# Optimization experiments

Measured on AMD Instinct MI355X. Metric: run time of the kernel, lower is better.

Reference implementation:

```python
import jax, jax.numpy as jnp
import numpy as np

N_USERS = 65536
N_ENT = 8192
C = 64
N_REL = 16
E = 1000000
NNZ = 1000000
LAMBDA_COEFF = 0.5
EPS = 1e-12


def setup_inputs() -> dict:
    key = jax.random.key(0)
    ks = jax.random.split(key, 8)
    return {
        "user_emb": jax.random.normal(ks[0], (N_USERS, C), jnp.float32) * 0.1,
        "entity_emb": jax.random.normal(ks[1], (N_ENT, C), jnp.float32) * 0.1,
        "weight": jax.random.normal(ks[2], (N_REL - 1, C), jnp.float32) * 0.1,
        "edge_index": jax.random.randint(ks[3], (2, E), 0, N_ENT, dtype=jnp.int32),
        "edge_type": jax.random.randint(ks[4], (E,), 1, N_REL, dtype=jnp.int32),
        "interact_rows": jax.random.randint(ks[5], (NNZ,), 0, N_USERS, dtype=jnp.int32),
        "interact_cols": jax.random.randint(ks[6], (NNZ,), 0, N_ENT, dtype=jnp.int32),
        "interact_vals": jax.random.uniform(ks[7], (NNZ,), jnp.float32),
        "n_hops": 2,
        "topk": 10,
    }


def _l2_normalize(x):
    # F.normalize(p=2, dim=1) with eps=1e-12
    n = jnp.linalg.norm(x, axis=-1, keepdims=True)
    return x / jnp.maximum(n, EPS)


def _build_adj_dense(context, topk):
    # cosine-sim kNN graph + symmetric normalization, returned dense [n, n]
    n = context.shape[0]
    cn = context / jnp.linalg.norm(context, axis=-1, keepdims=True)
    sim = cn @ cn.T                                  # [n, n]
    knn_val, knn_ind = jax.lax.top_k(sim, topk)      # [n, k]
    rowsum = knn_val.sum(-1)                         # sparse rowsum per row
    d = rowsum ** -0.5                               # D^{-1/2}
    vals = d[:, None] * knn_val * d[knn_ind]         # D^-1/2 A D^-1/2 values
    rows = jnp.broadcast_to(jnp.arange(n)[:, None], (n, topk))
    return jnp.zeros((n, n), context.dtype).at[rows, knn_ind].add(vals)


def _aggregate(entity_emb, user_emb, head, tail, edge_type,
               interact_rows, interact_cols, interact_vals, weight):
    rel = weight[edge_type - 1]                      # [E, C]
    neigh = entity_emb[tail] * rel                   # [E, C]
    # per-edge attention: (||h*r||_2 * ||t*r||_2)^2  -> scalar per edge
    s = (jnp.linalg.norm(entity_emb[head] * rel, axis=1)
         * jnp.linalg.norm(neigh, axis=1)) ** 2      # [E]
    # scatter_softmax over edges grouped by head
    smax = jax.ops.segment_max(s, head, num_segments=N_ENT)
    ex = jnp.exp(s - smax[head])
    denom = jax.ops.segment_sum(ex, head, num_segments=N_ENT)
    w = ex / denom[head]                             # [E]
    entity_agg = jax.ops.segment_sum(neigh * w[:, None], head, num_segments=N_ENT)
    # user_agg = interact_mat @ entity_emb (sparse COO mm)
    user_agg = jax.ops.segment_sum(interact_vals[:, None] * entity_emb[interact_cols],
                                   interact_rows, num_segments=N_USERS)
    score = jax.nn.softmax(user_emb @ weight.T, axis=-1)   # [n_users, n_rel-1]
    user_agg = user_agg + (score @ weight) * user_agg
    return entity_agg, user_agg


def reference(user_emb, entity_emb, weight, edge_index, edge_type,
              interact_rows, interact_cols, interact_vals, n_hops, topk):
    head, tail = edge_index[0], edge_index[1]
    origin_item_adj = _build_adj_dense(entity_emb, topk)
    entity_res = entity_emb
    user_res = user_emb
    ent, usr = entity_emb, user_emb
    for _ in range(n_hops):
        ent, usr = _aggregate(ent, usr, head, tail, edge_type,
                              interact_rows, interact_cols, interact_vals, weight)
        ent = _l2_normalize(ent)
        usr = _l2_normalize(usr)
        entity_res = entity_res + ent
        user_res = user_res + usr
    item_adj = (1.0 - LAMBDA_COEFF) * _build_adj_dense(entity_res, topk) \
               + LAMBDA_COEFF * origin_item_adj
    return entity_res, user_res, item_adj
```

## Files before the change

### kernel.cpp

```cpp
#include <hip/hip_runtime.h>
#include <math.h>
#include <float.h>

#define N_USERS 65536
#define N_ENT   8192
#define CDIM    64
#define N_RELM1 15
#define E_EDGES 1000000
#define NNZV    1000000
#define TOPK    10
#define NCAND   12
#define EPSN    1e-12f

typedef float f32x4 __attribute__((ext_vector_type(4)));
typedef short short8 __attribute__((ext_vector_type(8)));

__device__ inline unsigned umaxu(unsigned a, unsigned b){ return a > b ? a : b; }
__device__ inline unsigned uminu(unsigned a, unsigned b){ return a < b ? a : b; }

__device__ inline float wred_sum(float v){
#pragma unroll
  for (int m = 32; m; m >>= 1) v += __shfl_xor(v, m, 64);
  return v;
}
__device__ inline float wred_max(float v){
#pragma unroll
  for (int m = 32; m; m >>= 1) v = fmaxf(v, __shfl_xor(v, m, 64));
  return v;
}

__device__ inline unsigned bf16_rne(float x){
  unsigned u = __float_as_uint(x);
  return (u + 0x7FFFu + ((u >> 16) & 1u)) >> 16;
}

__global__ void k_rownorm_split(const float* __restrict__ x, float* __restrict__ cn,
                                short* __restrict__ hi_p, short* __restrict__ lo_p, int n){
  int w = (blockIdx.x * blockDim.x + threadIdx.x) >> 6;
  int k = threadIdx.x & 63;
  if (w >= n) return;
  float v = x[w * CDIM + k];
  float ss = wred_sum(v * v);
  float cv = v / sqrtf(ss);
  cn[w * CDIM + k] = cv;
  unsigned h = bf16_rne(cv);
  float hf = __uint_as_float(h << 16);
  unsigned l2 = bf16_rne(cv - hf);
  int T = w >> 4, c = w & 15;
  int f = k >> 5, q = (k >> 3) & 3, j = k & 7;
  size_t a = ((size_t)(T * 2 + f) * 64 + q * 16 + c) * 8 + j;
  hi_p[a] = (short)h;
  lo_p[a] = (short)l2;
}

__global__ __launch_bounds__(256) void k_sim_topk(const short* __restrict__ hi_p,
                                                  const short* __restrict__ lo_p,
                                                  unsigned* __restrict__ keys){
  const int tid = threadIdx.x;
  const int w = tid >> 6, l = tid & 63;
  const int c = l & 15, q = l >> 4;
  const int rowset = (w >> 1) << 4;
  const int half = w & 1;
  const int cy = blockIdx.y;
  const int row0 = blockIdx.x * 32 + rowset;
  const int R = row0 >> 4;

  const short8* H8 = (const short8*)hi_p;
  const short8* L8 = (const short8*)lo_p;

  const short8 a_hi0 = H8[(size_t)R * 128 + l];
  const short8 a_hi1 = H8[(size_t)R * 128 + 64 + l];
  const short8 a_lo0 = L8[(size_t)R * 128 + l];
  const short8 a_lo1 = L8[(size_t)R * 128 + 64 + l];

  unsigned key[4][8];
#pragma unroll
  for (int s = 0; s < 4; ++s)
#pragma unroll
    for (int t = 0; t < 8; ++t) key[s][t] = 0u;

  const f32x4 z4 = {0.f, 0.f, 0.f, 0.f};
  const int bt = cy * 256 + half * 128;
#pragma unroll 2
  for (int lt = 0; lt < 128; ++lt){
    const size_t bo = (size_t)(bt + lt) * 128 + l;
    short8 b_hi0 = H8[bo];
    short8 b_hi1 = H8[bo + 64];
    short8 b_lo0 = L8[bo];
    short8 b_lo1 = L8[bo + 64];
    f32x4 p0 = __builtin_amdgcn_mfma_f32_16x16x32_bf16(a_hi0, b_hi0, z4, 0, 0, 0);
    f32x4 p1 = __builtin_amdgcn_mfma_f32_16x16x32_bf16(a_hi0, b_lo0, z4, 0, 0, 0);
    f32x4 p2 = __builtin_amdgcn_mfma_f32_16x16x32_bf16(a_lo0, b_hi0, z4, 0, 0, 0);
    p0 = __builtin_amdgcn_mfma_f32_16x16x32_bf16(a_hi1, b_hi1, p0, 0, 0, 0);
    p1 = __builtin_amdgcn_mfma_f32_16x16x32_bf16(a_hi1, b_lo1, p1, 0, 0, 0);
    p2 = __builtin_amdgcn_mfma_f32_16x16x32_bf16(a_lo1, b_hi1, p2, 0, 0, 0);
#pragma unroll
    for (int s = 0; s < 4; ++s){
      float v = p0[s] + p1[s] + p2[s];
      unsigned u = __float_as_uint(v);
      unsigned kk = ((u ^ (unsigned)(((int)u >> 31) | 0x80000000)) & 0xFFFFFF00u) | (unsigned)lt;
#pragma unroll
      for (int i = 7; i >= 1; --i)
        key[s][i] = umaxu(uminu(key[s][i - 1], kk), key[s][i]);
      key[s][0] = umaxu(key[s][0], kk);
    }
  }

#pragma unroll
  for (int s = 0; s < 4; ++s){
    int grow = row0 + 4 * q + s;
    unsigned* kp = keys + ((size_t)grow * 64 + (size_t)(cy * 32 + half * 16 + c)) * 8;
    ((uint4*)kp)[0] = (uint4){key[s][0], key[s][1], key[s][2], key[s][3]};
    ((uint4*)kp)[1] = (uint4){key[s][4], key[s][5], key[s][6], key[s][7]};
  }
}

__global__ __launch_bounds__(256) void k_refine(const float* __restrict__ cn,
                                                const unsigned* __restrict__ keys,
                                                float* __restrict__ kv, int* __restrict__ ki,
                                                float* __restrict__ dvec){
  int row = blockIdx.x * 4 + (threadIdx.x >> 6);
  int l = threadIdx.x & 63;
  const unsigned* kp = keys + ((size_t)row * 64 + l) * 8;
  uint4 k0 = ((const uint4*)kp)[0], k1 = ((const uint4*)kp)[1];
  unsigned kk0 = k0.x, kk1 = k0.y, kk2 = k0.z, kk3 = k0.w;
  unsigned kk4 = k1.x, kk5 = k1.y, kk6 = k1.z, kk7 = k1.w;
  const int cbase = (l >> 5) * 4096 + ((l >> 4) & 1) * 2048 + (l & 15);

  int ji[NCAND];
#pragma unroll
  for (int t = 0; t < NCAND; ++t){
    unsigned bk = kk0;
    int myc = cbase + (int)(kk0 & 0xFFu) * 16;
    int bc = myc;
#pragma unroll
    for (int m = 32; m; m >>= 1){
      unsigned ok = (unsigned)__shfl_xor((int)bk, m, 64);
      int oc = __shfl_xor(bc, m, 64);
      if (ok > bk || (ok == bk && oc < bc)){ bk = ok; bc = oc; }
    }
    if (kk0 == bk && myc == bc){
      kk0 = kk1; kk1 = kk2; kk2 = kk3; kk3 = kk4; kk4 = kk5; kk5 = kk6; kk6 = kk7; kk7 = 0u;
    }
    ji[t] = bc;
  }

  float v = cn[(size_t)row * CDIM + l];
  float dv[NCAND];
#pragma unroll
  for (int t = 0; t < NCAND; ++t)
    dv[t] = wred_sum(v * cn[(size_t)ji[t] * CDIM + l]);

  unsigned used = 0;
  float rs = 0.f;
  for (int k = 0; k < TOPK; ++k){
    float bv = -FLT_MAX; int bi = 0x7FFFFFFF; int bs = 0;
#pragma unroll
    for (int t = 0; t < NCAND; ++t){
      if (used & (1u << t)) continue;
      if (dv[t] > bv || (dv[t] == bv && ji[t] < bi)){ bv = dv[t]; bi = ji[t]; bs = t; }
    }
    used |= 1u << bs; rs += bv;
    if (l == 0){ kv[(size_t)row * TOPK + k] = bv; ki[(size_t)row * TOPK + k] = bi; }
  }
  if (l == 0) dvec[row] = 1.0f / sqrtf(rs);
}

__global__ void k_hist(const int* __restrict__ keys, int* __restrict__ deg, int n){
  int e = blockIdx.x * blockDim.x + threadIdx.x;
  if (e < n) atomicAdd(&deg[keys[e]], 1);
}
__global__ __launch_bounds__(1024) void k_scan_local(const int* __restrict__ deg,
                                                     int* __restrict__ out,
                                                     int* __restrict__ part){
  __shared__ int sh[1024];
  int tid = threadIdx.x, g = blockIdx.x * 1024 + tid;
  int v = deg[g];
  sh[tid] = v; __syncthreads();
  for (int off = 1; off < 1024; off <<= 1){
    int t = (tid >= off) ? sh[tid - off] : 0;
    __syncthreads();
    sh[tid] += t;
    __syncthreads();
  }
  out[g] = sh[tid] - v;
  if (tid == 1023) part[blockIdx.x] = sh[1023];
}
__global__ void k_scan_part(int* __restrict__ part, int* __restrict__ total_out, int nb){
  int tid = threadIdx.x;
  int v = (tid < nb) ? part[tid] : 0;
  int orig = v;
  for (int off = 1; off < 64; off <<= 1){
    int t = __shfl_up(v, off, 64);
    if (tid >= off) v += t;
  }
  if (tid < nb) part[tid] = v - orig;
  if (tid == 63) *total_out = v;
}
__global__ __launch_bounds__(1024) void k_scan_add(int* __restrict__ out, const int* __restrict__ part){
  int g = blockIdx.x * 1024 + threadIdx.x;
  out[g] += part[blockIdx.x];
}
__global__ void k_scatter_graph(const int* __restrict__ head, const int* __restrict__ tail,
                                const int* __restrict__ etype, const int* __restrict__ rowptr,
                                int* __restrict__ cnt, int* __restrict__ pack, int n){
  int e = blockIdx.x * blockDim.x + threadIdx.x;
  if (e >= n) return;
  int h = head[e];
  int pos = rowptr[h] + atomicAdd(&cnt[h], 1);
  pack[pos] = tail[e] | ((etype[e] - 1) << 16);
}
__global__ void k_scatter_int(const int* __restrict__ rows, const int* __restrict__ cols,
                              const float* __restrict__ vals, const int* __restrict__ rowptr,
                              int* __restrict__ cnt, int* __restrict__ ocol,
                              float* __restrict__ oval, int n){
  int e = blockIdx.x * blockDim.x + threadIdx.x;
  if (e >= n) return;
  int r = rows[e];
  int pos = rowptr[r] + atomicAdd(&cnt[r], 1);
  ocol[pos] = cols[e];
  oval[pos] = vals[e];
}

__global__ __launch_bounds__(256) void k_normsq(const float* __restrict__ ent,
                                                const float* __restrict__ wmat,
                                                float* __restrict__ nsq){
  __shared__ float wl[N_RELM1 * CDIM];
  int tid = threadIdx.x;
  for (int t = tid; t < N_RELM1 * CDIM; t += 256) wl[t] = wmat[t];
  __syncthreads();
  int i = blockIdx.x * 4 + (tid >> 6);
  int lane = tid & 63;
  float v = ent[(size_t)i * CDIM + lane];
  float out = 0.f;
  for (int r = 0; r < N_RELM1; ++r){
    float t = v * wl[r * CDIM + lane];
    float ss = wred_sum(t * t);
    if (lane == r) out = ss;
  }
  if (lane < N_RELM1) nsq[i * N_RELM1 + lane] = out;
}

__global__ __launch_bounds__(256) void k_entity_hop(const float* __restrict__ ent_cur,
                                                    const float* __restrict__ nsq,
                                                    const float* __restrict__ wmat,
                                                    const int* __restrict__ rowptr,
                                                    const int* __restrict__ pack,
                                                    float* __restrict__ ent_next,
                                                    float* __restrict__ res, int hop0){
  __shared__ float wl[N_RELM1 * CDIM];
  int tid = threadIdx.x;
  for (int t = tid; t < N_RELM1 * CDIM; t += 256) wl[t] = wmat[t];
  __syncthreads();
  int i = blockIdx.x * 4 + (tid >> 6);
  int lane = tid & 63;
  int beg = rowptr[i], end = rowptr[i + 1];

  float sm = 0.f;
  for (int p = beg + lane; p < end; p += 64){
    int pk = pack[p]; int t = pk & 0xFFFF; int r = pk >> 16;
    sm = fmaxf(sm, nsq[i * N_RELM1 + r] * nsq[t * N_RELM1 + r]);
  }
  sm = wred_max(sm);

  float acc = 0.f, denom = 0.f;
  for (int p = beg; p < end; ++p){
    int pk = pack[p]; int t = pk & 0xFFFF; int r = pk >> 16;
    float s = nsq[i * N_RELM1 + r] * nsq[t * N_RELM1 + r];
    float e = expf(s - sm);
    denom += e;
    acc = fmaf(e * wl[r * CDIM + lane], ent_cur[(size_t)t * CDIM + lane], acc);
  }
  float agg = (end > beg) ? acc / denom : 0.f;
  float nrm = sqrtf(wred_sum(agg * agg));
  float out = agg / fmaxf(nrm, EPSN);
  if (hop0){
    ent_next[(size_t)i * CDIM + lane] = out;
    res[(size_t)i * CDIM + lane] = ent_cur[(size_t)i * CDIM + lane] + out;
  } else {
    res[(size_t)i * CDIM + lane] += out;
  }
}

__global__ __launch_bounds__(256) void k_user_hop(const float* __restrict__ base,
                                                  const float* __restrict__ ent_cur,
                                                  const float* __restrict__ wmat,
                                                  const int* __restrict__ rowptr,
                                                  const int* __restrict__ cols,
                                                  const float* __restrict__ vals,
                                                  float* __restrict__ res, int hop0){
  __shared__ float wl[N_RELM1 * CDIM];
  int tid = threadIdx.x;
  for (int t = tid; t < N_RELM1 * CDIM; t += 256) wl[t] = wmat[t];
  __syncthreads();
  int u = blockIdx.x * 4 + (tid >> 6);
  int lane = tid & 63;
  float bv = base[(size_t)u * CDIM + lane];
  float rprev = hop0 ? bv : res[(size_t)u * CDIM + lane];
  float uv = hop0 ? bv : (rprev - bv);

  float dr[N_RELM1];
#pragma unroll
  for (int r = 0; r < N_RELM1; ++r) dr[r] = wred_sum(uv * wl[r * CDIM + lane]);
  float mx = dr[0];
#pragma unroll
  for (int r = 1; r < N_RELM1; ++r) mx = fmaxf(mx, dr[r]);
  float se = 0.f;
#pragma unroll
  for (int r = 0; r < N_RELM1; ++r){ dr[r] = expf(dr[r] - mx); se += dr[r]; }
  float m = 0.f;
#pragma unroll
  for (int r = 0; r < N_RELM1; ++r) m = fmaf(dr[r], wl[r * CDIM + lane], m);
  m /= se;

  int beg = rowptr[u], end = rowptr[u + 1];
  float acc = 0.f;
  for (int p = beg; p < end; ++p)
    acc = fmaf(vals[p], ent_cur[(size_t)cols[p] * CDIM + lane], acc);

  float u2 = acc * (1.f + m);
  float nrm = sqrtf(wred_sum(u2 * u2));
  float out = u2 / fmaxf(nrm, EPSN);
  res[(size_t)u * CDIM + lane] = rprev + out;
}

__global__ void k_scatter_adj(const float* __restrict__ kv, const int* __restrict__ ki,
                              const float* __restrict__ d, float* __restrict__ adj,
                              float coef, int use_atomic){
  int g = blockIdx.x * blockDim.x + threadIdx.x;
  if (g >= N_ENT * TOPK) return;
  int i = g / TOPK;
  int j = ki[g];
  float v = coef * d[i] * kv[g] * d[j];
  if (use_atomic) atomicAdd(&adj[(size_t)i * N_ENT + j], v);
  else            adj[(size_t)i * N_ENT + j] = v;
}

extern "C" void kernel_launch(void* const* d_in, const int* in_sizes, int n_in,
                              void* d_out, int out_size, void* d_ws, size_t ws_size,
                              hipStream_t stream){
  const float* user_emb   = (const float*)d_in[0];
  const float* entity_emb = (const float*)d_in[1];
  const float* weight     = (const float*)d_in[2];
  const int*   head       = (const int*)d_in[3];
  const int*   tail       = head + E_EDGES;
  const int*   etype      = (const int*)d_in[4];
  const int*   irows      = (const int*)d_in[5];
  const int*   icols      = (const int*)d_in[6];
  const float* ivals      = (const float*)d_in[7];

  float* out_ent = (float*)d_out;
  float* out_usr = out_ent + (size_t)N_ENT * CDIM;
  float* out_adj = out_usr + (size_t)N_USERS * CDIM;

  char* W = (char*)d_ws;
  size_t off = 0;
  auto alloc = [&](size_t bytes) -> char* {
    char* p = W + off;
    off = (off + bytes + 1023) & ~(size_t)1023;
    return p;
  };
  float* cn       = (float*)alloc((size_t)N_ENT * CDIM * 4);
  short* cn_hi    = (short*)alloc((size_t)N_ENT * CDIM * 2);
  short* cn_lo    = (short*)alloc((size_t)N_ENT * CDIM * 2);
  unsigned* skeys = (unsigned*)alloc((size_t)N_ENT * 64 * 8 * 4);
  float* kv0      = (float*)alloc((size_t)N_ENT * TOPK * 4);
  int*   ki0      = (int*)  alloc((size_t)N_ENT * TOPK * 4);
  float* kv2      = (float*)alloc((size_t)N_ENT * TOPK * 4);
  int*   ki2      = (int*)  alloc((size_t)N_ENT * TOPK * 4);
  float* d0       = (float*)alloc((size_t)N_ENT * 4);
  float* d2       = (float*)alloc((size_t)N_ENT * 4);
  float* nsq      = (float*)alloc((size_t)N_ENT * N_RELM1 * 4);
  float* ent_a    = (float*)alloc((size_t)N_ENT * CDIM * 4);
  int*   grp_rowptr = (int*)alloc((size_t)(N_ENT + 1) * 4);
  int*   grp_cnt    = (int*)alloc((size_t)N_ENT * 4);
  int*   grp_pack   = (int*)alloc((size_t)E_EDGES * 4);
  int*   int_rowptr = (int*)alloc((size_t)(N_USERS + 1) * 4);
  int*   int_cnt    = (int*)alloc((size_t)N_USERS * 4);
  int*   int_col    = (int*)alloc((size_t)NNZV * 4);
  float* int_val    = (float*)alloc((size_t)NNZV * 4);
  int*   scan_part  = (int*)alloc(256);

  const int EB = (E_EDGES + 255) / 256;

  hipMemsetAsync(grp_cnt, 0, N_ENT * 4, stream);
  k_hist<<<EB, 256, 0, stream>>>(head, grp_cnt, E_EDGES);
  k_scan_local<<<N_ENT / 1024, 1024, 0, stream>>>(grp_cnt, grp_rowptr, scan_part);
  k_scan_part<<<1, 64, 0, stream>>>(scan_part, grp_rowptr + N_ENT, N_ENT / 1024);
  k_scan_add<<<N_ENT / 1024, 1024, 0, stream>>>(grp_rowptr, scan_part);
  hipMemsetAsync(grp_cnt, 0, N_ENT * 4, stream);
  k_scatter_graph<<<EB, 256, 0, stream>>>(head, tail, etype, grp_rowptr, grp_cnt, grp_pack, E_EDGES);

  hipMemsetAsync(int_cnt, 0, N_USERS * 4, stream);
  k_hist<<<EB, 256, 0, stream>>>(irows, int_cnt, NNZV);
  k_scan_local<<<N_USERS / 1024, 1024, 0, stream>>>(int_cnt, int_rowptr, scan_part);
  k_scan_part<<<1, 64, 0, stream>>>(scan_part, int_rowptr + N_USERS, N_USERS / 1024);
  k_scan_add<<<N_USERS / 1024, 1024, 0, stream>>>(int_rowptr, scan_part);
  hipMemsetAsync(int_cnt, 0, N_USERS * 4, stream);
  k_scatter_int<<<EB, 256, 0, stream>>>(irows, icols, ivals, int_rowptr, int_cnt, int_col, int_val, NNZV);

  k_rownorm_split<<<N_ENT / 4, 256, 0, stream>>>(entity_emb, cn, cn_hi, cn_lo, N_ENT);
  k_sim_topk<<<dim3(N_ENT / 32, 2), 256, 0, stream>>>(cn_hi, cn_lo, skeys);
  k_refine<<<N_ENT / 4, 256, 0, stream>>>(cn, skeys, kv0, ki0, d0);

  k_normsq<<<N_ENT / 4, 256, 0, stream>>>(entity_emb, weight, nsq);
  k_entity_hop<<<N_ENT / 4, 256, 0, stream>>>(entity_emb, nsq, weight, grp_rowptr, grp_pack, ent_a, out_ent, 1);
  k_user_hop<<<N_USERS / 4, 256, 0, stream>>>(user_emb, entity_emb, weight, int_rowptr, int_col, int_val, out_usr, 1);

  k_normsq<<<N_ENT / 4, 256, 0, stream>>>(ent_a, weight, nsq);
  k_entity_hop<<<N_ENT / 4, 256, 0, stream>>>(ent_a, nsq, weight, grp_rowptr, grp_pack, ent_a, out_ent, 0);
  k_user_hop<<<N_USERS / 4, 256, 0, stream>>>(user_emb, ent_a, weight, int_rowptr, int_col, int_val, out_usr, 0);

  k_rownorm_split<<<N_ENT / 4, 256, 0, stream>>>(out_ent, cn, cn_hi, cn_lo, N_ENT);
  k_sim_topk<<<dim3(N_ENT / 32, 2), 256, 0, stream>>>(cn_hi, cn_lo, skeys);
  k_refine<<<N_ENT / 4, 256, 0, stream>>>(cn, skeys, kv2, ki2, d2);

  hipMemsetAsync(out_adj, 0, (size_t)N_ENT * N_ENT * 4, stream);
  k_scatter_adj<<<(N_ENT * TOPK + 255) / 256, 256, 0, stream>>>(kv0, ki0, d0, out_adj, 0.5f, 0);
  k_scatter_adj<<<(N_ENT * TOPK + 255) / 256, 256, 0, stream>>>(kv2, ki2, d2, out_adj, 0.5f, 1);
}
```

Before: 1.125 ms.

## Fuse CSR builds, normsq into prep/hop kernels, and parallelize entity edge loop

Merges the two CSR constructions (histogram, scan, scatter) into single combined launches, folds the per-relation norm computation into the row-normalize kernel and into the first entity hop's epilogue, and merges the two adjacency scatters into one atomic kernel. The entity hop now loads 64 edges per wave in parallel and broadcasts them via shuffles instead of every lane reading each edge serially, and uses fast __expf. The aim is fewer launches and less serialized memory latency in the edge aggregation; fast exp and the change in atomic summation order can shift numerics slightly.

Result: faster. 1.032 ms (-8.2%).

```diff
diff --git a/kernel.cpp b/kernel.cpp
--- a/kernel.cpp
+++ b/kernel.cpp
@@ -34,11 +34,18 @@
   return (u + 0x7FFFu + ((u >> 16) & 1u)) >> 16;
 }
 
-__global__ void k_rownorm_split(const float* __restrict__ x, float* __restrict__ cn,
-                                short* __restrict__ hi_p, short* __restrict__ lo_p, int n){
-  int w = (blockIdx.x * blockDim.x + threadIdx.x) >> 6;
-  int k = threadIdx.x & 63;
-  if (w >= n) return;
+__global__ __launch_bounds__(256) void k_prep(const float* __restrict__ x, float* __restrict__ cn,
+                                              short* __restrict__ hi_p, short* __restrict__ lo_p,
+                                              const float* __restrict__ wmat, float* __restrict__ nsq,
+                                              int do_nsq){
+  __shared__ float wl[N_RELM1 * CDIM];
+  int tid = threadIdx.x;
+  if (do_nsq){
+    for (int t = tid; t < N_RELM1 * CDIM; t += 256) wl[t] = wmat[t];
+  }
+  __syncthreads();
+  int w = blockIdx.x * 4 + (tid >> 6);
+  int k = tid & 63;
   float v = x[w * CDIM + k];
   float ss = wred_sum(v * v);
   float cv = v / sqrtf(ss);
@@ -51,6 +58,15 @@
   size_t a = ((size_t)(T * 2 + f) * 64 + q * 16 + c) * 8 + j;
   hi_p[a] = (short)h;
   lo_p[a] = (short)l2;
+  if (do_nsq){
+    float out = 0.f;
+    for (int r = 0; r < N_RELM1; ++r){
+      float t = v * wl[r * CDIM + k];
+      float s2 = wred_sum(t * t);
+      if (k == r) out = s2;
+    }
+    if (k < N_RELM1) nsq[w * N_RELM1 + k] = out;
+  }
 }
 
 __global__ __launch_bounds__(256) void k_sim_topk(const short* __restrict__ hi_p,
@@ -166,16 +182,21 @@
   if (l == 0) dvec[row] = 1.0f / sqrtf(rs);
 }
 
-__global__ void k_hist(const int* __restrict__ keys, int* __restrict__ deg, int n){
+__global__ void k_hist2(const int* __restrict__ head, const int* __restrict__ irows,
+                        int* __restrict__ cnt_all){
   int e = blockIdx.x * blockDim.x + threadIdx.x;
-  if (e < n) atomicAdd(&deg[keys[e]], 1);
-}
-__global__ __launch_bounds__(1024) void k_scan_local(const int* __restrict__ deg,
-                                                     int* __restrict__ out,
-                                                     int* __restrict__ part){
+  if (e < E_EDGES)                  atomicAdd(&cnt_all[head[e]], 1);
+  else if (e < E_EDGES + NNZV)      atomicAdd(&cnt_all[N_ENT + irows[e - E_EDGES]], 1);
+}
+
+__global__ __launch_bounds__(1024) void k_scan_local2(const int* __restrict__ cnt_all,
+                                                      int* __restrict__ rp_grp,
+                                                      int* __restrict__ rp_int,
+                                                      int* __restrict__ part){
   __shared__ int sh[1024];
-  int tid = threadIdx.x, g = blockIdx.x * 1024 + tid;
-  int v = deg[g];
+  int b = blockIdx.x, tid = threadIdx.x;
+  int src = (b < 8) ? (b * 1024 + tid) : (N_ENT + (b - 8) * 1024 + tid);
+  int v = cnt_all[src];
   sh[tid] = v; __syncthreads();
   for (int off = 1; off < 1024; off <<= 1){
     int t = (tid >= off) ? sh[tid - off] : 0;
@@ -183,62 +204,61 @@
     sh[tid] += t;
     __syncthreads();
   }
-  out[g] = sh[tid] - v;
-  if (tid == 1023) part[blockIdx.x] = sh[1023];
-}
-__global__ void k_scan_part(int* __restrict__ part, int* __restrict__ total_out, int nb){
-  int tid = threadIdx.x;
-  int v = (tid < nb) ? part[tid] : 0;
-  int orig = v;
-  for (int off = 1; off < 64; off <<= 1){
-    int t = __shfl_up(v, off, 64);
-    if (tid >= off) v += t;
-  }
-  if (tid < nb) part[tid] = v - orig;
-  if (tid == 63) *total_out = v;
-}
-__global__ __launch_bounds__(1024) void k_scan_add(int* __restrict__ out, const int* __restrict__ part){
-  int g = blockIdx.x * 1024 + threadIdx.x;
-  out[g] += part[blockIdx.x];
-}
-__global__ void k_scatter_graph(const int* __restrict__ head, const int* __restrict__ tail,
-                                const int* __restrict__ etype, const int* __restrict__ rowptr,
-                                int* __restrict__ cnt, int* __restrict__ pack, int n){
+  int ex = sh[tid] - v;
+  if (b < 8) rp_grp[b * 1024 + tid] = ex;
+  else       rp_int[(b - 8) * 1024 + tid] = ex;
+  if (tid == 1023) part[b] = sh[1023];
+}
+
+__global__ void k_scan_part2(int* __restrict__ part){
+  int wid = threadIdx.x >> 6, lane = threadIdx.x & 63;
+  if (wid == 0){
+    int v = (lane < 8) ? part[lane] : 0;
+    int orig = v;
+    for (int off = 1; off < 64; off <<= 1){ int t = __shfl_up(v, off, 64); if (lane >= off) v += t; }
+    if (lane < 8) part[lane] = v - orig;
+  } else {
+    int v = part[8 + lane];
+    int orig = v;
+    for (int off = 1; off < 64; off <<= 1){ int t = __shfl_up(v, off, 64); if (lane >= off) v += t; }
+    part[8 + lane] = v - orig;
+  }
+}
+
+__global__ __launch_bounds__(1024) void k_scan_add2(int* __restrict__ rp_grp, int* __restrict__ rp_int,
+                                                    const int* __restrict__ part,
+                                                    int* __restrict__ wk_grp, int* __restrict__ wk_int){
+  int b = blockIdx.x, tid = threadIdx.x;
+  if (b < 8){
+    int g = b * 1024 + tid;
+    int v = rp_grp[g] + part[b];
+    rp_grp[g] = v; wk_grp[g] = v;
+  } else {
+    int g = (b - 8) * 1024 + tid;
+    int v = rp_int[g] + part[b];
+    rp_int[g] = v; wk_int[g] = v;
+  }
+  if (b == 0 && tid == 0){ rp_grp[N_ENT] = E_EDGES; rp_int[N_USERS] = NNZV; }
+}
+
+__global__ void k_scatter2(const int* __restrict__ head, const int* __restrict__ tail,
+                           const int* __restrict__ etype,
+                           const int* __restrict__ irows, const int* __restrict__ icols,
+                           const float* __restrict__ ivals,
+                           int* __restrict__ wk_grp, int* __restrict__ wk_int,
+                           int* __restrict__ pack, int* __restrict__ ocol, float* __restrict__ oval){
   int e = blockIdx.x * blockDim.x + threadIdx.x;
-  if (e >= n) return;
-  int h = head[e];
-  int pos = rowptr[h] + atomicAdd(&cnt[h], 1);
-  pack[pos] = tail[e] | ((etype[e] - 1) << 16);
-}
-__global__ void k_scatter_int(const int* __restrict__ rows, const int* __restrict__ cols,
-                              const float* __restrict__ vals, const int* __restrict__ rowptr,
-                              int* __restrict__ cnt, int* __restrict__ ocol,
-                              float* __restrict__ oval, int n){
-  int e = blockIdx.x * blockDim.x + threadIdx.x;
-  if (e >= n) return;
-  int r = rows[e];
-  int pos = rowptr[r] + atomicAdd(&cnt[r], 1);
-  ocol[pos] = cols[e];
-  oval[pos] = vals[e];
-}
-
-__global__ __launch_bounds__(256) void k_normsq(const float* __restrict__ ent,
-                                                const float* __restrict__ wmat,
-                                                float* __restrict__ nsq){
-  __shared__ float wl[N_RELM1 * CDIM];
-  int tid = threadIdx.x;
-  for (int t = tid; t < N_RELM1 * CDIM; t += 256) wl[t] = wmat[t];
-  __syncthreads();
-  int i = blockIdx.x * 4 + (tid >> 6);
-  int lane = tid & 63;
-  float v = ent[(size_t)i * CDIM + lane];
-  float out = 0.f;
-  for (int r = 0; r < N_RELM1; ++r){
-    float t = v * wl[r * CDIM + lane];
-    float ss = wred_sum(t * t);
-    if (lane == r) out = ss;
-  }
-  if (lane < N_RELM1) nsq[i * N_RELM1 + lane] = out;
+  if (e < E_EDGES){
+    int h = head[e];
+    int pos = atomicAdd(&wk_grp[h], 1);
+    pack[pos] = tail[e] | ((etype[e] - 1) << 16);
+  } else if (e < E_EDGES + NNZV){
+    int ee = e - E_EDGES;
+    int r = irows[ee];
+    int pos = atomicAdd(&wk_int[r], 1);
+    ocol[pos] = icols[ee];
+    oval[pos] = ivals[ee];
+  }
 }
 
 __global__ __launch_bounds__(256) void k_entity_hop(const float* __restrict__ ent_cur,
@@ -247,6 +267,7 @@
                                                     const int* __restrict__ rowptr,
                                                     const int* __restrict__ pack,
                                                     float* __restrict__ ent_next,
+                                                    float* __restrict__ nsq_next,
                                                     float* __restrict__ res, int hop0){
   __shared__ float wl[N_RELM1 * CDIM];
   int tid = threadIdx.x;
@@ -263,20 +284,38 @@
   }
   sm = wred_max(sm);
 
-  float acc = 0.f, denom = 0.f;
-  for (int p = beg; p < end; ++p){
-    int pk = pack[p]; int t = pk & 0xFFFF; int r = pk >> 16;
+  float acc = 0.f, dsum = 0.f;
+  for (int base = beg; base < end; base += 64){
+    int p = base + lane;
+    int pk = (p < end) ? pack[p] : 0;
+    int t = pk & 0xFFFF; int r = pk >> 16;
     float s = nsq[i * N_RELM1 + r] * nsq[t * N_RELM1 + r];
-    float e = expf(s - sm);
-    denom += e;
-    acc = fmaf(e * wl[r * CDIM + lane], ent_cur[(size_t)t * CDIM + lane], acc);
-  }
+    float e = (p < end) ? __expf(s - sm) : 0.f;
+    dsum += e;
+    int cnt = end - base; if (cnt > 64) cnt = 64;
+#pragma unroll 8
+    for (int qq = 0; qq < cnt; ++qq){
+      float eq = __shfl(e, qq, 64);
+      int tq = __shfl(t, qq, 64);
+      int rq = __shfl(r, qq, 64);
+      acc = fmaf(eq * wl[rq * CDIM + lane], ent_cur[(size_t)tq * CDIM + lane], acc);
+    }
+  }
+  float denom = wred_sum(dsum);
+
   float agg = (end > beg) ? acc / denom : 0.f;
   float nrm = sqrtf(wred_sum(agg * agg));
   float out = agg / fmaxf(nrm, EPSN);
   if (hop0){
     ent_next[(size_t)i * CDIM + lane] = out;
     res[(size_t)i * CDIM + lane] = ent_cur[(size_t)i * CDIM + lane] + out;
+    float o = 0.f;
+    for (int r = 0; r < N_RELM1; ++r){
+      float t = out * wl[r * CDIM + lane];
+      float s2 = wred_sum(t * t);
+      if (lane == r) o = s2;
+    }
+    if (lane < N_RELM1) nsq_next[i * N_RELM1 + lane] = o;
   } else {
     res[(size_t)i * CDIM + lane] += out;
   }
@@ -307,7 +346,7 @@
   for (int r = 1; r < N_RELM1; ++r) mx = fmaxf(mx, dr[r]);
   float se = 0.f;
 #pragma unroll
-  for (int r = 0; r < N_RELM1; ++r){ dr[r] = expf(dr[r] - mx); se += dr[r]; }
+  for (int r = 0; r < N_RELM1; ++r){ dr[r] = __expf(dr[r] - mx); se += dr[r]; }
   float m = 0.f;
 #pragma unroll
   for (int r = 0; r < N_RELM1; ++r) m = fmaf(dr[r], wl[r * CDIM + lane], m);
@@ -315,6 +354,7 @@
 
   int beg = rowptr[u], end = rowptr[u + 1];
   float acc = 0.f;
+#pragma unroll 4
   for (int p = beg; p < end; ++p)
     acc = fmaf(vals[p], ent_cur[(size_t)cols[p] * CDIM + lane], acc);
 
@@ -324,16 +364,21 @@
   res[(size_t)u * CDIM + lane] = rprev + out;
 }
 
-__global__ void k_scatter_adj(const float* __restrict__ kv, const int* __restrict__ ki,
-                              const float* __restrict__ d, float* __restrict__ adj,
-                              float coef, int use_atomic){
+__global__ void k_scatter_adj2(const float* __restrict__ kv0, const int* __restrict__ ki0,
+                               const float* __restrict__ d0,
+                               const float* __restrict__ kv2, const int* __restrict__ ki2,
+                               const float* __restrict__ d2,
+                               float* __restrict__ adj){
   int g = blockIdx.x * blockDim.x + threadIdx.x;
-  if (g >= N_ENT * TOPK) return;
-  int i = g / TOPK;
-  int j = ki[g];
-  float v = coef * d[i] * kv[g] * d[j];
-  if (use_atomic) atomicAdd(&adj[(size_t)i * N_ENT + j], v);
-  else            adj[(size_t)i * N_ENT + j] = v;
+  const int n = N_ENT * TOPK;
+  if (g < n){
+    int i = g / TOPK; int j = ki0[g];
+    atomicAdd(&adj[(size_t)i * N_ENT + j], 0.5f * d0[i] * kv0[g] * d0[j]);
+  } else if (g < 2 * n){
+    int gg = g - n;
+    int i = gg / TOPK; int j = ki2[gg];
+    atomicAdd(&adj[(size_t)i * N_ENT + j], 0.5f * d2[i] * kv2[gg] * d2[j]);
+  }
 }
 
 extern "C" void kernel_launch(void* const* d_in, const int* in_sizes, int n_in,
@@ -370,52 +415,48 @@
   int*   ki2      = (int*)  alloc((size_t)N_ENT * TOPK * 4);
   float* d0       = (float*)alloc((size_t)N_ENT * 4);
   float* d2       = (float*)alloc((size_t)N_ENT * 4);
-  float* nsq      = (float*)alloc((size_t)N_ENT * N_RELM1 * 4);
+  float* nsq_a    = (float*)alloc((size_t)N_ENT * N_RELM1 * 4);
+  float* nsq_b    = (float*)alloc((size_t)N_ENT * N_RELM1 * 4);
   float* ent_a    = (float*)alloc((size_t)N_ENT * CDIM * 4);
-  int*   grp_rowptr = (int*)alloc((size_t)(N_ENT + 1) * 4);
-  int*   grp_cnt    = (int*)alloc((size_t)N_ENT * 4);
-  int*   grp_pack   = (int*)alloc((size_t)E_EDGES * 4);
-  int*   int_rowptr = (int*)alloc((size_t)(N_USERS + 1) * 4);
-  int*   int_cnt    = (int*)alloc((size_t)N_USERS * 4);
-  int*   int_col    = (int*)alloc((size_t)NNZV * 4);
-  float* int_val    = (float*)alloc((size_t)NNZV * 4);
-  int*   scan_part  = (int*)alloc(256);
-
-  const int EB = (E_EDGES + 255) / 256;
-
-  hipMemsetAsync(grp_cnt, 0, N_ENT * 4, stream);
-  k_hist<<<EB, 256, 0, stream>>>(head, grp_cnt, E_EDGES);
-  k_scan_local<<<N_ENT / 1024, 1024, 0, stream>>>(grp_cnt, grp_rowptr, scan_part);
-  k_scan_part<<<1, 64, 0, stream>>>(scan_part, grp_rowptr + N_ENT, N_ENT / 1024);
-  k_scan_add<<<N_ENT / 1024, 1024, 0, stream>>>(grp_rowptr, scan_part);
-  hipMemsetAsync(grp_cnt, 0, N_ENT * 4, stream);
-  k_scatter_graph<<<EB, 256, 0, stream>>>(head, tail, etype, grp_rowptr, grp_cnt, grp_pack, E_EDGES);
-
-  hipMemsetAsync(int_cnt, 0, N_USERS * 4, stream);
-  k_hist<<<EB, 256, 0, stream>>>(irows, int_cnt, NNZV);
-  k_scan_local<<<N_USERS / 1024, 1024, 0, stream>>>(int_cnt, int_rowptr, scan_part);
-  k_scan_part<<<1, 64, 0, stream>>>(scan_part, int_rowptr + N_USERS, N_USERS / 1024);
-  k_scan_add<<<N_USERS / 1024, 1024, 0, stream>>>(int_rowptr, scan_part);
-  hipMemsetAsync(int_cnt, 0, N_USERS * 4, stream);
-  k_scatter_int<<<EB, 256, 0, stream>>>(irows, icols, ivals, int_rowptr, int_cnt, int_col, int_val, NNZV);
-
-  k_rownorm_split<<<N_ENT / 4, 256, 0, stream>>>(entity_emb, cn, cn_hi, cn_lo, N_ENT);
+  int*   cnt_all  = (int*)  alloc((size_t)(N_ENT + N_USERS) * 4);
+  int*   rp_grp   = (int*)  alloc((size_t)(N_ENT + 1) * 4);
+  int*   wk_grp   = (int*)  alloc((size_t)N_ENT * 4);
+  int*   grp_pack = (int*)  alloc((size_t)E_EDGES * 4);
+  int*   rp_int   = (int*)  alloc((size_t)(N_USERS + 1) * 4);
+  int*   wk_int   = (int*)  alloc((size_t)N_USERS * 4);
+  int*   int_col  = (int*)  alloc((size_t)NNZV * 4);
+  float* int_val  = (float*)alloc((size_t)NNZV * 4);
+  int*   part     = (int*)  alloc(128 * 4);
+
+  const int TOT = E_EDGES + NNZV;
+  const int TB  = (TOT + 255) / 256;
+
+  hipMemsetAsync(cnt_all, 0, (size_t)(N_ENT + N_USERS) * 4, stream);
+  k_hist2<<<TB, 256, 0, stream>>>(head, irows, cnt_all);
+  k_scan_local2<<<72, 1024, 0, stream>>>(cnt_all, rp_grp, rp_int, part);
+  k_scan_part2<<<1, 128, 0, stream>>>(part);
+  k_scan_add2<<<72, 1024, 0, stream>>>(rp_grp, rp_int, part, wk_grp, wk_int);
+  k_scatter2<<<TB, 256, 0, stream>>>(head, tail, etype, irows, icols, ivals,
+                                     wk_grp, wk_int, grp_pack, int_col, int_val);
+
+  k_prep<<<N_ENT / 4, 256, 0, stream>>>(entity_emb, cn, cn_hi, cn_lo, weight, nsq_a, 1);
   k_sim_topk<<<dim3(N_ENT / 32, 2), 256, 0, stream>>>(cn_hi, cn_lo, skeys);
   k_refine<<<N_ENT / 4, 256, 0, stream>>>(cn, skeys, kv0, ki0, d0);
 
-  k_normsq<<<N_ENT / 4, 256, 0, stream>>>(entity_emb, weight, nsq);
-  k_entity_hop<<<N_ENT / 4, 256, 0, stream>>>(entity_emb, nsq, weight, grp_rowptr, grp_pack, ent_a, out_ent, 1);
-  k_user_hop<<<N_USERS / 4, 256, 0, stream>>>(user_emb, entity_emb, weight, int_rowptr, int_col, int_val, out_usr, 1);
-
-  k_normsq<<<N_ENT / 4, 256, 0, stream>>>(ent_a, weight, nsq);
-  k_entity_hop<<<N_ENT / 4, 256, 0, stream>>>(ent_a, nsq, weight, grp_rowptr, grp_pack, ent_a, out_ent, 0);
-  k_user_hop<<<N_USERS / 4, 256, 0, stream>>>(user_emb, ent_a, weight, int_rowptr, int_col, int_val, out_usr, 0);
-
-  k_rownorm_split<<<N_ENT / 4, 256, 0, stream>>>(out_ent, cn, cn_hi, cn_lo, N_ENT);
+  k_entity_hop<<<N_ENT / 4, 256, 0, stream>>>(entity_emb, nsq_a, weight, rp_grp, grp_pack,
+                                              ent_a, nsq_b, out_ent, 1);
+  k_user_hop<<<N_USERS / 4, 256, 0, stream>>>(user_emb, entity_emb, weight, rp_int,
+                                              int_col, int_val, out_usr, 1);
+
+  k_entity_hop<<<N_ENT / 4, 256, 0, stream>>>(ent_a, nsq_b, weight, rp_grp, grp_pack,
+                                              ent_a, nsq_b, out_ent, 0);
+  k_user_hop<<<N_USERS / 4, 256, 0, stream>>>(user_emb, ent_a, weight, rp_int,
+                                              int_col, int_val, out_usr, 0);
+
+  k_prep<<<N_ENT / 4, 256, 0, stream>>>(out_ent, cn, cn_hi, cn_lo, weight, nsq_a, 0);
   k_sim_topk<<<dim3(N_ENT / 32, 2), 256, 0, stream>>>(cn_hi, cn_lo, skeys);
   k_refine<<<N_ENT / 4, 256, 0, stream>>>(cn, skeys, kv2, ki2, d2);
 
   hipMemsetAsync(out_adj, 0, (size_t)N_ENT * N_ENT * 4, stream);
-  k_scatter_adj<<<(N_ENT * TOPK + 255) / 256, 256, 0, stream>>>(kv0, ki0, d0, out_adj, 0.5f, 0);
-  k_scatter_adj<<<(N_ENT * TOPK + 255) / 256, 256, 0, stream>>>(kv2, ki2, d2, out_adj, 0.5f, 1);
-}
+  k_scatter_adj2<<<(2 * N_ENT * TOPK + 255) / 256, 256, 0, stream>>>(kv0, ki0, d0, kv2, ki2, d2, out_adj);
+}
```
